# Kernel optimization log

Measured on AMD Instinct MI355X. Metric: run time of the kernel, lower is better.

Reference implementation:

```python
import jax, jax.numpy as jnp
import numpy as np

N, K, IN_DIM, OUT_DIM = 131072, 16, 256, 128


def setup_inputs() -> dict:
    key = jax.random.key(0)
    ks = jax.random.split(key, 6)
    s1 = 1.0 / np.sqrt(IN_DIM)
    s2 = 1.0 / np.sqrt(OUT_DIM)
    return {
        "x": jax.random.normal(ks[0], (N, IN_DIM), dtype=jnp.float32),
        "z": jax.random.randint(ks[1], (N,), 0, K, dtype=jnp.int32),
        "W1": jax.random.uniform(ks[2], (K, IN_DIM, OUT_DIM), jnp.float32, -s1, s1),
        "b1": jax.random.uniform(ks[3], (K, OUT_DIM), jnp.float32, -s1, s1),
        "W2": jax.random.uniform(ks[4], (K, OUT_DIM, 2), jnp.float32, -s2, s2),
        "b2": jax.random.uniform(ks[5], (K, 2), jnp.float32, -s2, s2),
    }


def reference(x, z, W1, b1, W2, b2):
    # Per-cluster expert MLP: tokens with z==i go through expert i.
    # Loop over the fixed, small number of experts (k); data dims stay vectorized.
    k = W1.shape[0]
    ri = jnp.zeros((x.shape[0], 2), dtype=x.dtype)
    for i in range(k):
        h = jax.nn.relu(x @ W1[i] + b1[i])          # [N, out_dim]
        logits = h @ W2[i] + b2[i]                  # [N, 2]
        ri = jnp.where((z == i)[:, None], logits, ri)
    # Every z in [0, k) is covered, so every row of ri has been written
    # (matches the torch path where non-empty clusters overwrite -inf).
    return jax.nn.softmax(ri, axis=-1)
```

## Files before the change

kernel.cpp:

```cpp
#include <hip/hip_runtime.h>
#include <hip/hip_bf16.h>

#define KEXP   16
#define IN_DIM 256
#define OUT_DIM 128
#define TILE   128
#define BPE    16

typedef float f32x4 __attribute__((ext_vector_type(4)));
typedef short bf16x8 __attribute__((ext_vector_type(8)));
typedef const unsigned int __attribute__((address_space(1)))* gptr_t;
typedef unsigned int __attribute__((address_space(3)))* lptr_t;

__device__ __forceinline__ ushort f2bf(float f) {
    union { float f; unsigned u; } v; v.f = f;
    return (ushort)((v.u + 0x7fffu + ((v.u >> 16) & 1u)) >> 16);
}

__global__ __launch_bounds__(256) void prep_k(const float* __restrict__ W1,
                                              ushort* __restrict__ w1t,
                                              const int* __restrict__ z,
                                              int* __restrict__ counts, int n) {
    __shared__ float ld[64][65];
    int bid = blockIdx.x, tid = threadIdx.x;
    if (bid < 128) {
        int e = bid >> 3, sub = bid & 7;
        int k0 = (sub & 3) * 64, n0 = (sub >> 2) * 64;
        const float* src = W1 + (long)e * (IN_DIM * OUT_DIM);
        int tr = tid >> 6, tc = tid & 63;
#pragma unroll
        for (int i = 0; i < 16; i++) {
            int row = i * 4 + tr;
            ld[row][tc] = src[(k0 + row) * OUT_DIM + n0 + tc];
        }
        __syncthreads();
        char* dst = (char*)w1t + (long)e * (OUT_DIM * IN_DIM * 2);
#pragma unroll
        for (int i = 0; i < 16; i++) {
            int col = n0 + i * 4 + tr;
            int L = (col * IN_DIM + k0 + tc) * 2;
            int S = L ^ ((col & 7) << 4);
            *(ushort*)(dst + S) = f2bf(ld[tc][i * 4 + tr]);
        }
    } else {
        int* h = (int*)ld;
        if (tid < KEXP) h[tid] = 0;
        __syncthreads();
        for (int i = (bid - 128) * 256 + tid; i < n; i += 256 * 256)
            atomicAdd(&h[z[i]], 1);
        __syncthreads();
        if (tid < KEXP) atomicAdd(&counts[tid], h[tid]);
    }
}

__global__ void scan_k(const int* __restrict__ counts, int* __restrict__ bases) {
    int li = threadIdx.x & 63;
    int c = (li < KEXP) ? counts[li] : 0;
    int v = c;
#pragma unroll
    for (int d = 1; d < KEXP; d <<= 1) {
        int t = __shfl_up(v, d, 64);
        if (li >= d) v += t;
    }
    if (li < KEXP) bases[li] = v - c;
}

__global__ __launch_bounds__(256) void scatter_k(const int* __restrict__ z,
                                                 const int* __restrict__ bases,
                                                 int* __restrict__ cursors,
                                                 int* __restrict__ perm, int n) {
    __shared__ int lc[KEXP];
    __shared__ int lb[KEXP];
    int tid = threadIdx.x;
    if (tid < KEXP) lc[tid] = 0;
    __syncthreads();
    int base = blockIdx.x * 1024 + tid;
    int e[4], r[4];
#pragma unroll
    for (int j = 0; j < 4; j++) {
        int i = base + j * 256;
        if (i < n) {
            e[j] = z[i];
            r[j] = atomicAdd(&lc[e[j]], 1);
        } else e[j] = -1;
    }
    __syncthreads();
    if (tid < KEXP && lc[tid] > 0) lb[tid] = atomicAdd(&cursors[tid], lc[tid]);
    __syncthreads();
#pragma unroll
    for (int j = 0; j < 4; j++) {
        int i = base + j * 256;
        if (i < n) perm[bases[e[j]] + lb[e[j]] + r[j]] = i;
    }
}

__global__ __launch_bounds__(512, 1) void mlp_k(
    const float* __restrict__ x, const float* __restrict__ b1,
    const float* __restrict__ W2, const float* __restrict__ b2,
    const int* __restrict__ counts, const int* __restrict__ bases,
    const int* __restrict__ perm, const ushort* __restrict__ w1t,
    float* __restrict__ out) {
    __shared__ char Wl[65536];
    __shared__ char Al[65536];

    int b = blockIdx.x;
    int e = b >> 4, slot = b & 15;
    int cnt = counts[e];
    int pb0 = bases[e];
    int ntiles = (cnt + TILE - 1) / TILE;

    int tid = threadIdx.x;
    int lane = tid & 63, w = tid >> 6;
    int li = lane & 15, q = lane >> 4;

    const char* wsrc = (const char*)w1t + (long)e * (OUT_DIM * IN_DIM * 2);
#pragma unroll
    for (int i = 0; i < 8; i++) {
        int off = w * 8192 + i * 1024;
        __builtin_amdgcn_global_load_lds((gptr_t)(wsrc + off + lane * 16),
                                         (lptr_t)(Wl + off), 16, 0, 0);
    }

    float bbv[8], w2a[8], w2b[8];
#pragma unroll
    for (int nn = 0; nn < 8; nn++) {
        int col = nn * 16 + li;
        bbv[nn] = b1[e * OUT_DIM + col];
        w2a[nn] = W2[(e * OUT_DIM + col) * 2 + 0];
        w2b[nn] = W2[(e * OUT_DIM + col) * 2 + 1];
    }
    float bb0 = b2[e * 2 + 0], bb1 = b2[e * 2 + 1];

    uint2 pk[16];
    int pb_cur = 0, nr_cur = 0;
    if (slot < ntiles) {
        pb_cur = pb0 + slot * TILE;
        nr_cur = cnt - slot * TILE;
        int rr = w * 16 + li;
        int pv = perm[pb_cur + (rr < nr_cur ? rr : nr_cur - 1)];
        f32x4 av[16];
#pragma unroll
        for (int i = 0; i < 16; i++) {
            int g = __shfl(pv, i, 16);
            av[i] = *(const f32x4*)((const char*)x + (long)g * 1024 + lane * 16);
        }
#pragma unroll
        for (int i = 0; i < 16; i++) {
            pk[i].x = (unsigned)f2bf(av[i][0]) | ((unsigned)f2bf(av[i][1]) << 16);
            pk[i].y = (unsigned)f2bf(av[i][2]) | ((unsigned)f2bf(av[i][3]) << 16);
        }
    }

    for (int t = slot; t < ntiles; t += BPE) {
#pragma unroll
        for (int i = 0; i < 16; i++) {
            int r = w * 16 + i;
            *(uint2*)(Al + r * 512 + ((lane * 8) ^ ((r & 7) << 4))) = pk[i];
        }
        __syncthreads();

        int tn = t + BPE;
        int pb_nx = 0, nr_nx = 0;
        f32x4 av[16];
        bool have_nx = (tn < ntiles);
        if (have_nx) {
            pb_nx = pb0 + tn * TILE;
            nr_nx = cnt - tn * TILE;
            int rr = w * 16 + li;
            int pv = perm[pb_nx + (rr < nr_nx ? rr : nr_nx - 1)];
#pragma unroll
            for (int i = 0; i < 16; i++) {
                int g = __shfl(pv, i, 16);
                av[i] = *(const f32x4*)((const char*)x + (long)g * 1024 + lane * 16);
            }
        }

        f32x4 acc[8];
#pragma unroll
        for (int nn = 0; nn < 8; nn++) acc[nn] = (f32x4)0.0f;

        int arow = w * 16 + li;
        int aswz = (arow & 7) << 4;
#pragma unroll
        for (int kk = 0; kk < 8; kk++) {
            bf16x8 af = *(const bf16x8*)(Al + arow * 512 + ((kk * 64 + q * 16) ^ aswz));
#pragma unroll
            for (int nn = 0; nn < 8; nn++) {
                int col = nn * 16 + li;
                bf16x8 bf = *(const bf16x8*)(Wl + col * 512 + ((kk * 64 + q * 16) ^ ((col & 7) << 4)));
                acc[nn] = __builtin_amdgcn_mfma_f32_16x16x32_bf16(af, bf, acc[nn], 0, 0, 0);
            }
        }

        float p0[4] = {0.f, 0.f, 0.f, 0.f}, p1[4] = {0.f, 0.f, 0.f, 0.f};
#pragma unroll
        for (int nn = 0; nn < 8; nn++) {
#pragma unroll
            for (int r = 0; r < 4; r++) {
                float h = fmaxf(acc[nn][r] + bbv[nn], 0.0f);
                p0[r] += h * w2a[nn];
                p1[r] += h * w2b[nn];
            }
        }
#pragma unroll
        for (int m = 1; m < 16; m <<= 1)
#pragma unroll
            for (int r = 0; r < 4; r++) {
                p0[r] += __shfl_xor(p0[r], m, 64);
                p1[r] += __shfl_xor(p1[r], m, 64);
            }
        if (li == 0) {
#pragma unroll
            for (int r = 0; r < 4; r++) {
                int mm = w * 16 + q * 4 + r;
                if (mm < nr_cur) {
                    int orig = perm[pb_cur + mm];
                    float l0 = p0[r] + bb0, l1 = p1[r] + bb1;
                    float mx = fmaxf(l0, l1);
                    float e0 = __expf(l0 - mx), e1 = __expf(l1 - mx);
                    float inv = 1.0f / (e0 + e1);
                    *(float2*)(out + (long)orig * 2) = make_float2(e0 * inv, e1 * inv);
                }
            }
        }

        if (have_nx) {
#pragma unroll
            for (int i = 0; i < 16; i++) {
                pk[i].x = (unsigned)f2bf(av[i][0]) | ((unsigned)f2bf(av[i][1]) << 16);
                pk[i].y = (unsigned)f2bf(av[i][2]) | ((unsigned)f2bf(av[i][3]) << 16);
            }
        }
        __syncthreads();
        pb_cur = pb_nx;
        nr_cur = nr_nx;
    }
}

extern "C" void kernel_launch(void* const* d_in, const int* in_sizes, int n_in,
                              void* d_out, int out_size, void* d_ws, size_t ws_size,
                              hipStream_t stream) {
    const float* x  = (const float*)d_in[0];
    const int*   z  = (const int*)d_in[1];
    const float* W1 = (const float*)d_in[2];
    const float* b1 = (const float*)d_in[3];
    const float* W2 = (const float*)d_in[4];
    const float* b2 = (const float*)d_in[5];
    float* out = (float*)d_out;
    int n = in_sizes[1];

    int* counts  = (int*)d_ws;
    int* cursors = counts + 16;
    int* basesp  = counts + 32;
    int* perm    = counts + 256;
    ushort* w1t  = (ushort*)((char*)d_ws + 1024 + (size_t)n * 4);

    hipMemsetAsync(counts, 0, 128, stream);
    prep_k<<<384, 256, 0, stream>>>(W1, w1t, z, counts, n);
    scan_k<<<1, 64, 0, stream>>>(counts, basesp);
    scatter_k<<<(n + 1023) / 1024, 256, 0, stream>>>(z, basesp, cursors, perm, n);
    mlp_k<<<KEXP * BPE, 512, 0, stream>>>(x, b1, W2, b2, counts, basesp, perm, w1t, out);
}
```

Before: 224.4 us.

## Fuse prep, scan, scatter and MLP into one cooperative kernel with grid syncs

Replaces the four separate launches (W1 transpose plus histogram, scan, scatter, MLP) with a single cooperative kernel of 256 blocks that uses grid.sync between phases. The aim is to remove per-launch overhead and the inter-kernel gaps. In the MLP loop, the perm index load for the next tile now issues before the LDS store and barrier, so its latency overlaps with them. The cost is three grid-wide barriers and a dependence on cooperative launch. The histogram and scatter now assume n is at most 256*512 elements, so larger inputs would be silently truncated.

```diff
diff --git a/kernel.cpp b/kernel.cpp
--- a/kernel.cpp
+++ b/kernel.cpp
@@ -1,11 +1,16 @@
 #include <hip/hip_runtime.h>
 #include <hip/hip_bf16.h>
+#include <hip/hip_cooperative_groups.h>
+
+namespace cg = cooperative_groups;
 
 #define KEXP   16
 #define IN_DIM 256
 #define OUT_DIM 128
 #define TILE   128
 #define BPE    16
+#define NBLK   256
+#define NTHR   512
 
 typedef float f32x4 __attribute__((ext_vector_type(4)));
 typedef short bf16x8 __attribute__((ext_vector_type(8)));
@@ -17,223 +22,217 @@
     return (ushort)((v.u + 0x7fffu + ((v.u >> 16) & 1u)) >> 16);
 }
 
-__global__ __launch_bounds__(256) void prep_k(const float* __restrict__ W1,
-                                              ushort* __restrict__ w1t,
-                                              const int* __restrict__ z,
-                                              int* __restrict__ counts, int n) {
-    __shared__ float ld[64][65];
+__global__ __launch_bounds__(NTHR, 1) void fused_k(
+    const float* __restrict__ x, const int* __restrict__ z,
+    const float* __restrict__ W1, const float* __restrict__ b1,
+    const float* __restrict__ W2, const float* __restrict__ b2,
+    float* __restrict__ out,
+    int* __restrict__ counts, int* __restrict__ cursors,
+    int* __restrict__ bases, int* __restrict__ perm,
+    ushort* __restrict__ w1t, int n) {
+    __shared__ __align__(16) char smem[131072];
+    cg::grid_group grid = cg::this_grid();
     int bid = blockIdx.x, tid = threadIdx.x;
-    if (bid < 128) {
+
+    {
+        float (*ld)[65] = (float(*)[65])smem;
+        int* shh = (int*)(smem + 73728);
+        if (tid < KEXP) shh[tid] = 0;
+        __syncthreads();
         int e = bid >> 3, sub = bid & 7;
         int k0 = (sub & 3) * 64, n0 = (sub >> 2) * 64;
-        const float* src = W1 + (long)e * (IN_DIM * OUT_DIM);
         int tr = tid >> 6, tc = tid & 63;
-#pragma unroll
-        for (int i = 0; i < 16; i++) {
-            int row = i * 4 + tr;
-            ld[row][tc] = src[(k0 + row) * OUT_DIM + n0 + tc];
-        }
-        __syncthreads();
-        char* dst = (char*)w1t + (long)e * (OUT_DIM * IN_DIM * 2);
-#pragma unroll
-        for (int i = 0; i < 16; i++) {
-            int col = n0 + i * 4 + tr;
-            int L = (col * IN_DIM + k0 + tc) * 2;
-            int S = L ^ ((col & 7) << 4);
-            *(ushort*)(dst + S) = f2bf(ld[tc][i * 4 + tr]);
-        }
-    } else {
-        int* h = (int*)ld;
-        if (tid < KEXP) h[tid] = 0;
-        __syncthreads();
-        for (int i = (bid - 128) * 256 + tid; i < n; i += 256 * 256)
-            atomicAdd(&h[z[i]], 1);
-        __syncthreads();
-        if (tid < KEXP) atomicAdd(&counts[tid], h[tid]);
-    }
-}
-
-__global__ void scan_k(const int* __restrict__ counts, int* __restrict__ bases) {
-    int li = threadIdx.x & 63;
-    int c = (li < KEXP) ? counts[li] : 0;
-    int v = c;
-#pragma unroll
-    for (int d = 1; d < KEXP; d <<= 1) {
-        int t = __shfl_up(v, d, 64);
-        if (li >= d) v += t;
-    }
-    if (li < KEXP) bases[li] = v - c;
-}
-
-__global__ __launch_bounds__(256) void scatter_k(const int* __restrict__ z,
-                                                 const int* __restrict__ bases,
-                                                 int* __restrict__ cursors,
-                                                 int* __restrict__ perm, int n) {
-    __shared__ int lc[KEXP];
-    __shared__ int lb[KEXP];
-    int tid = threadIdx.x;
-    if (tid < KEXP) lc[tid] = 0;
-    __syncthreads();
-    int base = blockIdx.x * 1024 + tid;
-    int e[4], r[4];
-#pragma unroll
-    for (int j = 0; j < 4; j++) {
-        int i = base + j * 256;
+        if (bid < 128 && tid < 256) {
+            const float* src = W1 + (long)e * (IN_DIM * OUT_DIM);
+#pragma unroll
+            for (int i = 0; i < 16; i++)
+                ld[i * 4 + tr][tc] = src[(k0 + i * 4 + tr) * OUT_DIM + n0 + tc];
+        }
+        if (tid >= 256) {
+            int t0 = bid * 512 + (tid - 256);
+            if (t0 < n)       atomicAdd(&shh[z[t0]], 1);
+            if (t0 + 256 < n) atomicAdd(&shh[z[t0 + 256]], 1);
+        }
+        __syncthreads();
+        if (bid < 128 && tid < 256) {
+            char* dst = (char*)w1t + (long)e * (OUT_DIM * IN_DIM * 2);
+#pragma unroll
+            for (int i = 0; i < 16; i++) {
+                int col = n0 + i * 4 + tr;
+                int L = (col * IN_DIM + k0 + tc) * 2;
+                *(ushort*)(dst + (L ^ ((col & 7) << 4))) = f2bf(ld[tc][i * 4 + tr]);
+            }
+        }
+        if (tid < KEXP) atomicAdd(&counts[tid], shh[tid]);
+    }
+    grid.sync();
+
+    if (bid == 0 && tid < 64) {
+        int c = (tid < KEXP) ? counts[tid] : 0;
+        int v = c;
+#pragma unroll
+        for (int d = 1; d < KEXP; d <<= 1) {
+            int t = __shfl_up(v, d, 64);
+            if (tid >= d) v += t;
+        }
+        if (tid < KEXP) bases[tid] = v - c;
+    }
+    grid.sync();
+
+    {
+        int* lc = (int*)smem;
+        int* lb = lc + 16;
+        if (tid < KEXP) lc[tid] = 0;
+        __syncthreads();
+        int i = bid * 512 + tid;
+        int e = -1, r = 0;
         if (i < n) {
-            e[j] = z[i];
-            r[j] = atomicAdd(&lc[e[j]], 1);
-        } else e[j] = -1;
-    }
-    __syncthreads();
-    if (tid < KEXP && lc[tid] > 0) lb[tid] = atomicAdd(&cursors[tid], lc[tid]);
-    __syncthreads();
-#pragma unroll
-    for (int j = 0; j < 4; j++) {
-        int i = base + j * 256;
-        if (i < n) perm[bases[e[j]] + lb[e[j]] + r[j]] = i;
-    }
-}
-
-__global__ __launch_bounds__(512, 1) void mlp_k(
-    const float* __restrict__ x, const float* __restrict__ b1,
-    const float* __restrict__ W2, const float* __restrict__ b2,
-    const int* __restrict__ counts, const int* __restrict__ bases,
-    const int* __restrict__ perm, const ushort* __restrict__ w1t,
-    float* __restrict__ out) {
-    __shared__ char Wl[65536];
-    __shared__ char Al[65536];
-
-    int b = blockIdx.x;
-    int e = b >> 4, slot = b & 15;
-    int cnt = counts[e];
-    int pb0 = bases[e];
-    int ntiles = (cnt + TILE - 1) / TILE;
-
-    int tid = threadIdx.x;
-    int lane = tid & 63, w = tid >> 6;
-    int li = lane & 15, q = lane >> 4;
-
-    const char* wsrc = (const char*)w1t + (long)e * (OUT_DIM * IN_DIM * 2);
-#pragma unroll
-    for (int i = 0; i < 8; i++) {
-        int off = w * 8192 + i * 1024;
-        __builtin_amdgcn_global_load_lds((gptr_t)(wsrc + off + lane * 16),
-                                         (lptr_t)(Wl + off), 16, 0, 0);
-    }
-
-    float bbv[8], w2a[8], w2b[8];
-#pragma unroll
-    for (int nn = 0; nn < 8; nn++) {
-        int col = nn * 16 + li;
-        bbv[nn] = b1[e * OUT_DIM + col];
-        w2a[nn] = W2[(e * OUT_DIM + col) * 2 + 0];
-        w2b[nn] = W2[(e * OUT_DIM + col) * 2 + 1];
-    }
-    float bb0 = b2[e * 2 + 0], bb1 = b2[e * 2 + 1];
-
-    uint2 pk[16];
-    int pb_cur = 0, nr_cur = 0;
-    if (slot < ntiles) {
-        pb_cur = pb0 + slot * TILE;
-        nr_cur = cnt - slot * TILE;
-        int rr = w * 16 + li;
-        int pv = perm[pb_cur + (rr < nr_cur ? rr : nr_cur - 1)];
-        f32x4 av[16];
-#pragma unroll
-        for (int i = 0; i < 16; i++) {
-            int g = __shfl(pv, i, 16);
-            av[i] = *(const f32x4*)((const char*)x + (long)g * 1024 + lane * 16);
-        }
-#pragma unroll
-        for (int i = 0; i < 16; i++) {
-            pk[i].x = (unsigned)f2bf(av[i][0]) | ((unsigned)f2bf(av[i][1]) << 16);
-            pk[i].y = (unsigned)f2bf(av[i][2]) | ((unsigned)f2bf(av[i][3]) << 16);
-        }
-    }
-
-    for (int t = slot; t < ntiles; t += BPE) {
-#pragma unroll
-        for (int i = 0; i < 16; i++) {
-            int r = w * 16 + i;
-            *(uint2*)(Al + r * 512 + ((lane * 8) ^ ((r & 7) << 4))) = pk[i];
-        }
-        __syncthreads();
-
-        int tn = t + BPE;
-        int pb_nx = 0, nr_nx = 0;
-        f32x4 av[16];
-        bool have_nx = (tn < ntiles);
-        if (have_nx) {
-            pb_nx = pb0 + tn * TILE;
-            nr_nx = cnt - tn * TILE;
+            e = z[i];
+            r = atomicAdd(&lc[e], 1);
+        }
+        __syncthreads();
+        if (tid < KEXP && lc[tid] > 0) lb[tid] = atomicAdd(&cursors[tid], lc[tid]);
+        __syncthreads();
+        if (e >= 0) perm[bases[e] + lb[e] + r] = i;
+    }
+    grid.sync();
+
+    {
+        char* Wl = smem;
+        char* Al = smem + 65536;
+        int b = bid;
+        int e = b >> 4, slot = b & 15;
+        int cnt = counts[e];
+        int pb0 = bases[e];
+        int ntiles = (cnt + TILE - 1) / TILE;
+
+        int lane = tid & 63, w = tid >> 6;
+        int li = lane & 15, q = lane >> 4;
+
+        const char* wsrc = (const char*)w1t + (long)e * (OUT_DIM * IN_DIM * 2);
+#pragma unroll
+        for (int i = 0; i < 8; i++) {
+            int off = w * 8192 + i * 1024;
+            __builtin_amdgcn_global_load_lds((gptr_t)(wsrc + off + lane * 16),
+                                             (lptr_t)(Wl + off), 16, 0, 0);
+        }
+
+        float bbv[8], w2a[8], w2b[8];
+#pragma unroll
+        for (int nn = 0; nn < 8; nn++) {
+            int col = nn * 16 + li;
+            bbv[nn] = b1[e * OUT_DIM + col];
+            w2a[nn] = W2[(e * OUT_DIM + col) * 2 + 0];
+            w2b[nn] = W2[(e * OUT_DIM + col) * 2 + 1];
+        }
+        float bb0 = b2[e * 2 + 0], bb1 = b2[e * 2 + 1];
+
+        uint2 pk[16];
+        int pb_cur = 0, nr_cur = 0;
+        if (slot < ntiles) {
+            pb_cur = pb0 + slot * TILE;
+            nr_cur = cnt - slot * TILE;
             int rr = w * 16 + li;
-            int pv = perm[pb_nx + (rr < nr_nx ? rr : nr_nx - 1)];
+            int pv = perm[pb_cur + (rr < nr_cur ? rr : nr_cur - 1)];
+            f32x4 av[16];
 #pragma unroll
             for (int i = 0; i < 16; i++) {
                 int g = __shfl(pv, i, 16);
                 av[i] = *(const f32x4*)((const char*)x + (long)g * 1024 + lane * 16);
             }
-        }
-
-        f32x4 acc[8];
-#pragma unroll
-        for (int nn = 0; nn < 8; nn++) acc[nn] = (f32x4)0.0f;
-
-        int arow = w * 16 + li;
-        int aswz = (arow & 7) << 4;
-#pragma unroll
-        for (int kk = 0; kk < 8; kk++) {
-            bf16x8 af = *(const bf16x8*)(Al + arow * 512 + ((kk * 64 + q * 16) ^ aswz));
-#pragma unroll
-            for (int nn = 0; nn < 8; nn++) {
-                int col = nn * 16 + li;
-                bf16x8 bf = *(const bf16x8*)(Wl + col * 512 + ((kk * 64 + q * 16) ^ ((col & 7) << 4)));
-                acc[nn] = __builtin_amdgcn_mfma_f32_16x16x32_bf16(af, bf, acc[nn], 0, 0, 0);
-            }
-        }
-
-        float p0[4] = {0.f, 0.f, 0.f, 0.f}, p1[4] = {0.f, 0.f, 0.f, 0.f};
-#pragma unroll
-        for (int nn = 0; nn < 8; nn++) {
-#pragma unroll
-            for (int r = 0; r < 4; r++) {
-                float h = fmaxf(acc[nn][r] + bbv[nn], 0.0f);
-                p0[r] += h * w2a[nn];
-                p1[r] += h * w2b[nn];
-            }
-        }
-#pragma unroll
-        for (int m = 1; m < 16; m <<= 1)
-#pragma unroll
-            for (int r = 0; r < 4; r++) {
-                p0[r] += __shfl_xor(p0[r], m, 64);
-                p1[r] += __shfl_xor(p1[r], m, 64);
-            }
-        if (li == 0) {
-#pragma unroll
-            for (int r = 0; r < 4; r++) {
-                int mm = w * 16 + q * 4 + r;
-                if (mm < nr_cur) {
-                    int orig = perm[pb_cur + mm];
-                    float l0 = p0[r] + bb0, l1 = p1[r] + bb1;
-                    float mx = fmaxf(l0, l1);
-                    float e0 = __expf(l0 - mx), e1 = __expf(l1 - mx);
-                    float inv = 1.0f / (e0 + e1);
-                    *(float2*)(out + (long)orig * 2) = make_float2(e0 * inv, e1 * inv);
-                }
-            }
-        }
-
-        if (have_nx) {
 #pragma unroll
             for (int i = 0; i < 16; i++) {
                 pk[i].x = (unsigned)f2bf(av[i][0]) | ((unsigned)f2bf(av[i][1]) << 16);
                 pk[i].y = (unsigned)f2bf(av[i][2]) | ((unsigned)f2bf(av[i][3]) << 16);
             }
         }
-        __syncthreads();
-        pb_cur = pb_nx;
-        nr_cur = nr_nx;
+
+        for (int t = slot; t < ntiles; t += BPE) {
+            int tn = t + BPE;
+            bool have_nx = (tn < ntiles);
+            int pb_nx = 0, nr_nx = 0, pv_nx = 0;
+            if (have_nx) {
+                pb_nx = pb0 + tn * TILE;
+                nr_nx = cnt - tn * TILE;
+                int rr = w * 16 + li;
+                pv_nx = perm[pb_nx + (rr < nr_nx ? rr : nr_nx - 1)];
+            }
+
+#pragma unroll
+            for (int i = 0; i < 16; i++) {
+                int r = w * 16 + i;
+                *(uint2*)(Al + r * 512 + ((lane * 8) ^ ((r & 7) << 4))) = pk[i];
+            }
+            __syncthreads();
+
+            f32x4 av[16];
+            if (have_nx) {
+#pragma unroll
+                for (int i = 0; i < 16; i++) {
+                    int g = __shfl(pv_nx, i, 16);
+                    av[i] = *(const f32x4*)((const char*)x + (long)g * 1024 + lane * 16);
+                }
+            }
+
+            f32x4 acc[8];
+#pragma unroll
+            for (int nn = 0; nn < 8; nn++) acc[nn] = (f32x4)0.0f;
+            int arow = w * 16 + li;
+            int aswz = (arow & 7) << 4;
+#pragma unroll
+            for (int kk = 0; kk < 8; kk++) {
+                bf16x8 af = *(const bf16x8*)(Al + arow * 512 + ((kk * 64 + q * 16) ^ aswz));
+#pragma unroll
+                for (int nn = 0; nn < 8; nn++) {
+                    int col = nn * 16 + li;
+                    bf16x8 bf = *(const bf16x8*)(Wl + col * 512 + ((kk * 64 + q * 16) ^ ((col & 7) << 4)));
+                    acc[nn] = __builtin_amdgcn_mfma_f32_16x16x32_bf16(af, bf, acc[nn], 0, 0, 0);
+                }
+            }
+
+            float p0[4] = {0.f, 0.f, 0.f, 0.f}, p1[4] = {0.f, 0.f, 0.f, 0.f};
+#pragma unroll
+            for (int nn = 0; nn < 8; nn++) {
+#pragma unroll
+                for (int r = 0; r < 4; r++) {
+                    float h = fmaxf(acc[nn][r] + bbv[nn], 0.0f);
+                    p0[r] += h * w2a[nn];
+                    p1[r] += h * w2b[nn];
+                }
+            }
+#pragma unroll
+            for (int m = 1; m < 16; m <<= 1)
+#pragma unroll
+                for (int r = 0; r < 4; r++) {
+                    p0[r] += __shfl_xor(p0[r], m, 64);
+                    p1[r] += __shfl_xor(p1[r], m, 64);
+                }
+            if (li == 0) {
+#pragma unroll
+                for (int r = 0; r < 4; r++) {
+                    int mm = w * 16 + q * 4 + r;
+                    if (mm < nr_cur) {
+                        int orig = perm[pb_cur + mm];
+                        float l0 = p0[r] + bb0, l1 = p1[r] + bb1;
+                        float mx = fmaxf(l0, l1);
+                        float e0 = __expf(l0 - mx), e1 = __expf(l1 - mx);
+                        float inv = 1.0f / (e0 + e1);
+                        *(float2*)(out + (long)orig * 2) = make_float2(e0 * inv, e1 * inv);
+                    }
+                }
+            }
+
+            if (have_nx) {
+#pragma unroll
+                for (int i = 0; i < 16; i++) {
+                    pk[i].x = (unsigned)f2bf(av[i][0]) | ((unsigned)f2bf(av[i][1]) << 16);
+                    pk[i].y = (unsigned)f2bf(av[i][2]) | ((unsigned)f2bf(av[i][3]) << 16);
+                }
+            }
+            __syncthreads();
+            pb_cur = pb_nx;
+            nr_cur = nr_nx;
+        }
     }
 }
 
@@ -256,8 +255,9 @@
     ushort* w1t  = (ushort*)((char*)d_ws + 1024 + (size_t)n * 4);
 
     hipMemsetAsync(counts, 0, 128, stream);
-    prep_k<<<384, 256, 0, stream>>>(W1, w1t, z, counts, n);
-    scan_k<<<1, 64, 0, stream>>>(counts, basesp);
-    scatter_k<<<(n + 1023) / 1024, 256, 0, stream>>>(z, basesp, cursors, perm, n);
-    mlp_k<<<KEXP * BPE, 512, 0, stream>>>(x, b1, W2, b2, counts, basesp, perm, w1t, out);
+
+    void* args[] = {(void*)&x, (void*)&z, (void*)&W1, (void*)&b1, (void*)&W2,
+                    (void*)&b2, (void*)&out, (void*)&counts, (void*)&cursors,
+                    (void*)&basesp, (void*)&perm, (void*)&w1t, (void*)&n};
+    hipLaunchCooperativeKernel((void*)fused_k, dim3(NBLK), dim3(NTHR), args, 0, stream);
 }
```

After: 320.2 us. 42.7% more time.
